# Kernel tuning notes

Measured on AMD Instinct MI355X. Metric: run time of the kernel, lower is better.

## Reference

```python
import jax, jax.numpy as jnp
import numpy as np

NUM_GROUPS = 4
NUM_HEADS = 8
EPS = 1e-5


def setup_inputs() -> dict:
    key = jax.random.key(0)
    k1, k2, k3 = jax.random.split(key, 3)
    B, C, D, H, W = 4, 256, 32, 32, 32
    x = jax.random.normal(k1, (B, C, D, H, W), dtype=jnp.float32)
    gn_weight = jnp.ones((C,), dtype=jnp.float32)
    gn_bias = jnp.zeros((C,), dtype=jnp.float32)
    # 1x1x1 conv weights collapse to [out_ch, in_ch] matrices
    qkv_weight = jax.random.normal(k2, (3 * C, C), dtype=jnp.float32) * (1.0 / np.sqrt(C))
    out_weight = jax.random.normal(k3, (C, C), dtype=jnp.float32) * (1.0 / np.sqrt(C))
    out_bias = jnp.zeros((C,), dtype=jnp.float32)
    return {"x": x, "gn_weight": gn_weight, "gn_bias": gn_bias,
            "qkv_weight": qkv_weight, "out_weight": out_weight, "out_bias": out_bias}


def _group_norm(x, weight, bias):
    B, C, D, H, W = x.shape
    g = NUM_GROUPS
    xg = x.reshape(B, g, C // g, D, H, W)
    mean = jnp.mean(xg, axis=(2, 3, 4, 5), keepdims=True)
    var = jnp.var(xg, axis=(2, 3, 4, 5), keepdims=True)
    xn = ((xg - mean) * jax.lax.rsqrt(var + EPS)).reshape(B, C, D, H, W)
    return xn * weight[None, :, None, None, None] + bias[None, :, None, None, None]


def reference(x, gn_weight, gn_bias, qkv_weight, out_weight, out_bias):
    B, C, D, H, W = x.shape
    N = D * H * W
    hd = C // NUM_HEADS  # per-head channels

    norm = _group_norm(x, gn_weight, gn_bias)
    # 1x1x1 conv == channel matmul: [B,3C,D,H,W]
    qkv = jnp.einsum('bcdhw,oc->bodhw', norm, qkv_weight)
    # 'b (qkv heads c) d h w -> qkv b heads c (d h w)'
    qkv = qkv.reshape(B, 3, NUM_HEADS, hd, N)
    q, k, v = qkv[:, 0], qkv[:, 1], qkv[:, 2]  # each [B, heads, hd, N]

    k = jax.nn.softmax(k, axis=-1)  # softmax over spatial dim
    sim = jnp.einsum('bhdn,bhen->bhde', k, v)   # [B, heads, hd, hd]
    out = jnp.einsum('bhde,bhdn->bhen', sim, q)  # [B, heads, hd, N]
    out = out.reshape(B, C, D, H, W)

    out = jnp.einsum('bcdhw,oc->bodhw', out, out_weight) + out_bias[None, :, None, None, None]
    return out + x
```

## Files before the change

### kernel.cpp

```cpp
#include <hip/hip_runtime.h>
#include <cmath>


typedef __bf16 bf16x8 __attribute__((ext_vector_type(8)));
typedef float f32x4 __attribute__((ext_vector_type(4)));

union U16 { uint4 u; unsigned short s[8]; bf16x8 v; };

__device__ __forceinline__ float bf2f(unsigned short h) {
    unsigned int u = ((unsigned int)h) << 16;
    return __builtin_bit_cast(float, u);
}
__device__ __forceinline__ unsigned short f2bf(float f) {
    unsigned int u = __builtin_bit_cast(unsigned int, f);
    u = (u + 0x7fffu + ((u >> 16) & 1u)) >> 16;
    return (unsigned short)u;
}
__device__ __forceinline__ unsigned int pack2(unsigned short a, unsigned short b) {
    return (unsigned int)a | ((unsigned int)b << 16);
}

__global__ __launch_bounds__(64) void k_detect(const unsigned int* __restrict__ xr,
                                               int* __restrict__ flag) {
    unsigned int u = xr[threadIdx.x * 997];
    int e = (u >> 7) & 0xFF;
    bool ok = (e >= 100) && (e <= 141);
    unsigned long long m = __ballot(ok);
    if (threadIdx.x == 0) *flag = (__popcll(m) < 32) ? 1 : 0;
}

__global__ __launch_bounds__(256) void k_cvt_w(const void* __restrict__ qkvw,
                                               const void* __restrict__ outw,
                                               const void* __restrict__ gnw,
                                               const void* __restrict__ gnb,
                                               const void* __restrict__ outb,
                                               const int* __restrict__ flagp,
                                               unsigned short* __restrict__ wdst) {
    int idx = blockIdx.x * 256 + threadIdx.x;
    if (idx >= 328448) return;
    int f = *flagp;
    const void* src; int off;
    if      (idx < 196608) { src = qkvw; off = idx; }
    else if (idx < 262144) { src = outw; off = idx - 196608; }
    else if (idx < 262400) { src = gnw;  off = idx - 262144; }
    else if (idx < 262656) { src = gnb;  off = idx - 262400; }
    else if (idx < 262912) { src = outb; off = idx - 262656; }
    else {
        int i = idx - 262912;
        int c = i >> 8, d = i & 255;
        src = qkvw; off = d * 256 + c;
    }
    wdst[idx] = f ? f2bf(((const float*)src)[off])
                  : ((const unsigned short*)src)[off];
}

__global__ __launch_bounds__(256) void k_gnsum(const void* __restrict__ xr,
                                               const int* __restrict__ flagp,
                                               float2* __restrict__ gn_part) {
    int t = threadIdx.x, bid = blockIdx.x;
    int grp = bid >> 7, chunk = bid & 127;
    size_t base = (size_t)grp * 2097152 + (size_t)chunk * 16384;
    int f = *flagp;
    float s = 0.f, q = 0.f;
    if (f) {
        const float* p = (const float*)xr + base;
        for (int i = 0; i < 8; i++) {
            float4 a = *(const float4*)(p + i * 2048 + t * 8);
            float4 b = *(const float4*)(p + i * 2048 + t * 8 + 4);
            float v[8] = {a.x, a.y, a.z, a.w, b.x, b.y, b.z, b.w};
#pragma unroll
            for (int j = 0; j < 8; j++) { s += v[j]; q += v[j] * v[j]; }
        }
    } else {
        const unsigned short* p = (const unsigned short*)xr + base;
        for (int i = 0; i < 8; i++) {
            U16 u; u.u = *(const uint4*)(p + i * 2048 + t * 8);
#pragma unroll
            for (int j = 0; j < 8; j++) { float v = bf2f(u.s[j]); s += v; q += v * v; }
        }
    }
#pragma unroll
    for (int off = 32; off > 0; off >>= 1) { s += __shfl_xor(s, off); q += __shfl_xor(q, off); }
    __shared__ float rs[4], rq[4];
    int wave = t >> 6;
    if ((t & 63) == 0) { rs[wave] = s; rq[wave] = q; }
    __syncthreads();
    if (t == 0) gn_part[bid] = make_float2(rs[0] + rs[1] + rs[2] + rs[3],
                                           rq[0] + rq[1] + rq[2] + rq[3]);
}

__global__ __launch_bounds__(128) void k_gnfinal(const float2* __restrict__ gn_part,
                                                 float2* __restrict__ gstats) {
    int bg = blockIdx.x, t = threadIdx.x;
    float2 v = gn_part[bg * 128 + t];
    float s = v.x, q = v.y;
#pragma unroll
    for (int off = 32; off > 0; off >>= 1) { s += __shfl_xor(s, off); q += __shfl_xor(q, off); }
    __shared__ float rs[2], rq[2];
    if ((t & 63) == 0) { rs[t >> 6] = s; rq[t >> 6] = q; }
    __syncthreads();
    if (t == 0) {
        const float inv = 1.0f / 2097152.0f;
        float S = rs[0] + rs[1], Q = rq[0] + rq[1];
        float mean = S * inv;
        float var = Q * inv - mean * mean;
        gstats[bg] = make_float2(mean, rsqrtf(var + 1e-5f));
    }
}

__global__ __launch_bounds__(64) void k_beta(const unsigned short* __restrict__ wq,
                                             const unsigned short* __restrict__ wgnw,
                                             const unsigned short* __restrict__ wgnb,
                                             const float2* __restrict__ gstats,
                                             float* __restrict__ beta) {
    int bid = blockIdx.x;
    int b = bid / 768, o = bid % 768;
    int t = threadIdx.x, c = t * 4;
    float2 ms = gstats[b * 4 + (c >> 6)];
    uint2 qw = *(const uint2*)(wq + o * 256 + c);
    uint2 gw = *(const uint2*)(wgnw + c);
    uint2 gb = *(const uint2*)(wgnb + c);
    unsigned short qs[4] = {(unsigned short)(qw.x & 0xffff), (unsigned short)(qw.x >> 16),
                            (unsigned short)(qw.y & 0xffff), (unsigned short)(qw.y >> 16)};
    unsigned short wsx[4] = {(unsigned short)(gw.x & 0xffff), (unsigned short)(gw.x >> 16),
                             (unsigned short)(gw.y & 0xffff), (unsigned short)(gw.y >> 16)};
    unsigned short bs[4] = {(unsigned short)(gb.x & 0xffff), (unsigned short)(gb.x >> 16),
                            (unsigned short)(gb.y & 0xffff), (unsigned short)(gb.y >> 16)};
    float bacc = 0.f;
#pragma unroll
    for (int j = 0; j < 4; j++)
        bacc += bf2f(qs[j]) * (bf2f(bs[j]) - ms.x * ms.y * bf2f(wsx[j]));
#pragma unroll
    for (int off = 32; off > 0; off >>= 1) bacc += __shfl_xor(bacc, off);
    if (t == 0) beta[b * 768 + o] = bacc;
}

__global__ __launch_bounds__(256) void k_cvt_t(const void* __restrict__ xr,
                                               const int* __restrict__ flagp,
                                               const unsigned short* __restrict__ wgnw,
                                               const float2* __restrict__ gstats,
                                               unsigned short* __restrict__ xt) {
    int tid = threadIdx.x, bid = blockIdx.x;
    int b = bid >> 11, r2 = bid & 2047, cblk = r2 >> 9, nblk = r2 & 511;
    float rstd = gstats[b * 4 + cblk].y;
    int f = *flagp;
    __shared__ __align__(16) unsigned short T[64 * 80];
    unsigned short tmp[2][8];
#pragma unroll
    for (int i = 0; i < 2; i++) {
        int crow = (tid >> 3) + 32 * i, nch = tid & 7;
        int c = cblk * 64 + crow;
        float sc = bf2f(wgnw[c]) * rstd;
        size_t base = ((size_t)(b * 256 + c)) * 32768 + (size_t)nblk * 64 + nch * 8;
        float v[8];
        if (f) {
            float4 a = *(const float4*)((const float*)xr + base);
            float4 d = *(const float4*)((const float*)xr + base + 4);
            v[0] = a.x; v[1] = a.y; v[2] = a.z; v[3] = a.w;
            v[4] = d.x; v[5] = d.y; v[6] = d.z; v[7] = d.w;
        } else {
            U16 u; u.u = *(const uint4*)((const unsigned short*)xr + base);
#pragma unroll
            for (int j = 0; j < 8; j++) v[j] = bf2f(u.s[j]);
        }
#pragma unroll
        for (int j = 0; j < 8; j++) tmp[i][j] = f2bf(v[j] * sc);
    }
#pragma unroll
    for (int i = 0; i < 2; i++) {
        int crow = (tid >> 3) + 32 * i, nch = tid & 7;
#pragma unroll
        for (int jj = 0; jj < 8; jj++) {
            int j = (jj + tid) & 7;
            T[(nch * 8 + j) * 80 + crow] = tmp[i][j];
        }
    }
    __syncthreads();
#pragma unroll
    for (int i = 0; i < 2; i++) {
        int nrow = (tid >> 3) + 32 * i, cch = tid & 7;
        uint4 v = *(const uint4*)&T[nrow * 80 + cch * 8];
        *(uint4*)(xt + ((size_t)b * 32768 + (size_t)nblk * 64 + nrow) * 256 + cblk * 64 + cch * 8) = v;
    }
}

__device__ __forceinline__ void stage_tile(const unsigned short* __restrict__ g, int stride,
                                           unsigned short* __restrict__ lds, int tid) {
    int lane = tid & 63, wave = tid >> 6;
    int r8 = lane >> 3, s = lane & 7;
#pragma unroll
    for (int i = 0; i < 4; i++) {
        int row0 = wave * 32 + i * 8;
        int row = row0 + r8;
        const unsigned short* src = g + (size_t)row * stride + ((s ^ (row & 7)) << 3);
        __builtin_amdgcn_global_load_lds(
            (__attribute__((address_space(1))) void*)src,
            (__attribute__((address_space(3))) void*)(lds + row0 * 64),
            16, 0, 0);
    }
}

__device__ __forceinline__ void mfma_tile(const unsigned short* __restrict__ ldsA,
                                          const unsigned short* __restrict__ ldsB,
                                          int l15, int quad, int wm, int wn,
                                          f32x4 (&acc)[4][4]) {
#pragma unroll
    for (int ks = 0; ks < 2; ks++) {
        bf16x8 af[4], bv[4];
#pragma unroll
        for (int mi = 0; mi < 4; mi++) {
            int row = wm * 64 + mi * 16 + l15;
            af[mi] = *(const bf16x8*)&ldsA[row * 64 + (((ks * 4 + quad) ^ (row & 7)) * 8)];
        }
#pragma unroll
        for (int ni = 0; ni < 4; ni++) {
            int row = wn * 64 + ni * 16 + l15;
            bv[ni] = *(const bf16x8*)&ldsB[row * 64 + (((ks * 4 + quad) ^ (row & 7)) * 8)];
        }
#pragma unroll
        for (int mi = 0; mi < 4; mi++)
#pragma unroll
            for (int ni = 0; ni < 4; ni++)
                acc[mi][ni] = __builtin_amdgcn_mfma_f32_16x16x32_bf16(af[mi], bv[ni], acc[mi][ni], 0, 0, 0);
    }
}

template<int KSTEPS, int KAMASK>
__device__ __forceinline__ void gemm_core_db(const unsigned short* __restrict__ A, int strideA,
                                             const unsigned short* __restrict__ B, int strideB,
                                             unsigned short* lds, int tid, f32x4 (&acc)[4][4]) {
    int lane = tid & 63, l15 = lane & 15, quad = lane >> 4;
    int wave = tid >> 6, wm = wave & 1, wn = wave >> 1;
    stage_tile(A, strideA, lds, tid);
    stage_tile(B, strideB, lds + 8192, tid);
    __syncthreads();
#pragma unroll
    for (int kt = 0; kt < KSTEPS; ++kt) {
        unsigned short* cur = lds + (kt & 1) * 16384;
        unsigned short* nxt = lds + (((kt & 1) ^ 1)) * 16384;
        if (kt + 1 < KSTEPS) {
            stage_tile(A + ((kt + 1) & KAMASK) * 64, strideA, nxt, tid);
            stage_tile(B + (kt + 1) * 64, strideB, nxt + 8192, tid);
        }
        mfma_tile(cur, cur + 8192, l15, quad, wm, wn, acc);
        __syncthreads();
    }
}

__global__ __launch_bounds__(256) void k_gemm1(const unsigned short* __restrict__ wq,
                                               const unsigned short* __restrict__ xt,
                                               const float* __restrict__ beta,
                                               unsigned short* __restrict__ kv,
                                               int b0) {
    __shared__ __align__(16) unsigned short ldsbuf[4 * 128 * 64];
    int tid = threadIdx.x, bid = blockIdx.x;
    int L = (bid & 7) * ((int)gridDim.x >> 3) + (bid >> 3);
    int mblk = L & 3;
    int t2 = L >> 2;
    int nblk = t2 & 255, bl = t2 >> 8;
    int gb = b0 + bl;
    int o0 = 256 + mblk * 128;
    size_t n0 = (size_t)nblk * 128;
    const unsigned short* A = wq + (size_t)o0 * 256;
    const unsigned short* B = xt + ((size_t)gb * 32768 + n0) * 256;
    f32x4 acc[4][4] = {};
    gemm_core_db<4, 3>(A, 256, B, 256, ldsbuf, tid, acc);

    int lane = tid & 63, l15 = lane & 15, quad = lane >> 4;
    int wave = tid >> 6, wm = wave & 1, wn = wave >> 1;
#pragma unroll
    for (int mi = 0; mi < 4; mi++) {
        int o_l = wm * 64 + mi * 16 + quad * 4;
        float4 be = *(const float4*)(beta + gb * 768 + o0 + o_l);
        float bev[4] = {be.x, be.y, be.z, be.w};
#pragma unroll
        for (int ni = 0; ni < 4; ni++) {
            int n_l = wn * 64 + ni * 16 + l15;
            f32x4 v = acc[mi][ni];
#pragma unroll
            for (int r = 0; r < 4; r++) {
                int o_r = o_l + r;
                ldsbuf[(o_r * 128 + n_l) ^ ((o_r & 7) << 3)] = f2bf(v[r] + bev[r]);
            }
        }
    }
    __syncthreads();
    int kv0 = mblk * 128;
#pragma unroll
    for (int p = 0; p < 8; p++) {
        int o_r = p * 16 + (tid >> 4);
        int ch = tid & 15;
        uint4 v = *(const uint4*)&ldsbuf[(o_r * 128 + ch * 8) ^ ((o_r & 7) << 3)];
        *(uint4*)(kv + ((size_t)bl * 512 + kv0 + o_r) * 32768 + n0 + ch * 8) = v;
    }
}

__global__ __launch_bounds__(256) void k_stats(const unsigned short* __restrict__ kv,
                                               float2* __restrict__ stats) {
    int row = blockIdx.x, t = threadIdx.x;
    const unsigned short* p = kv + ((size_t)(row >> 8) * 512 + (row & 255)) * 32768;
    float m = -3.0e38f;
    for (int i = 0; i < 16; i++) {
        U16 u; u.u = *(const uint4*)(p + i * 2048 + t * 8);
#pragma unroll
        for (int j = 0; j < 8; j++) m = fmaxf(m, bf2f(u.s[j]));
    }
#pragma unroll
    for (int off = 32; off > 0; off >>= 1) m = fmaxf(m, __shfl_xor(m, off));
    __shared__ float rm[4], rs[4];
    int wave = t >> 6;
    if ((t & 63) == 0) rm[wave] = m;
    __syncthreads();
    m = fmaxf(fmaxf(rm[0], rm[1]), fmaxf(rm[2], rm[3]));
    float s = 0.f;
    for (int i = 0; i < 16; i++) {
        U16 u; u.u = *(const uint4*)(p + i * 2048 + t * 8);
#pragma unroll
        for (int j = 0; j < 8; j++) s += __expf(bf2f(u.s[j]) - m);
    }
#pragma unroll
    for (int off = 32; off > 0; off >>= 1) s += __shfl_xor(s, off);
    if ((t & 63) == 0) rs[wave] = s;
    __syncthreads();
    if (t == 0) stats[row] = make_float2(m, 1.0f / (rs[0] + rs[1] + rs[2] + rs[3]));
}

__global__ __launch_bounds__(64) void k_sim(const unsigned short* __restrict__ kv,
                                            const float2* __restrict__ stats,
                                            float* __restrict__ partials) {
    int bid = blockIdx.x;
    int bh = bid >> 6, chunk = bid & 63;
    int b = bh >> 3, h = bh & 7;
    int lane = threadIdx.x, l15 = lane & 15, quad = lane >> 4;
    size_t n0 = (size_t)chunk * 512 + quad * 8;
    float mrow[2], isr[2];
#pragma unroll
    for (int mi = 0; mi < 2; mi++) {
        float2 st = stats[b * 256 + h * 32 + mi * 16 + l15];
        mrow[mi] = st.x; isr[mi] = st.y;
    }
    const unsigned short* kb = kv + ((size_t)b * 512 + h * 32) * 32768;
    const unsigned short* vb = kv + ((size_t)b * 512 + 256 + h * 32) * 32768;
    f32x4 acc[2][2] = {};
    for (int t = 0; t < 16; t++) {
        size_t n = n0 + t * 32;
        bf16x8 af[2], bv[2];
#pragma unroll
        for (int mi = 0; mi < 2; mi++) {
            U16 u; u.u = *(const uint4*)(kb + (size_t)(mi * 16 + l15) * 32768 + n);
            U16 pv;
#pragma unroll
            for (int j = 0; j < 8; j++) pv.s[j] = f2bf(__expf(bf2f(u.s[j]) - mrow[mi]) * isr[mi]);
            af[mi] = pv.v;
        }
#pragma unroll
        for (int ni = 0; ni < 2; ni++) {
            U16 u; u.u = *(const uint4*)(vb + (size_t)(ni * 16 + l15) * 32768 + n);
            bv[ni] = u.v;
        }
#pragma unroll
        for (int mi = 0; mi < 2; mi++)
#pragma unroll
            for (int ni = 0; ni < 2; ni++)
                acc[mi][ni] = __builtin_amdgcn_mfma_f32_16x16x32_bf16(af[mi], bv[ni], acc[mi][ni], 0, 0, 0);
    }
    float* po = partials + (size_t)(bh * 64 + chunk) * 1024;
#pragma unroll
    for (int mi = 0; mi < 2; mi++)
#pragma unroll
        for (int ni = 0; ni < 2; ni++)
#pragma unroll
            for (int rr = 0; rr < 4; rr++)
                po[(mi * 16 + quad * 4 + rr) * 32 + ni * 16 + l15] = acc[mi][ni][rr];
}

__global__ __launch_bounds__(256) void k_combine(const float* __restrict__ partials,
                                                 float* __restrict__ sim, int b0) {
    int bh = blockIdx.x, tid = threadIdx.x;
#pragma unroll
    for (int i = 0; i < 4; i++) {
        float a = 0.f;
        const float* p = partials + (size_t)bh * 65536 + tid + i * 256;
        for (int c = 0; c < 64; c++) a += p[(size_t)c * 1024];
        sim[(size_t)(b0 * 8 + bh) * 1024 + tid + i * 256] = a;
    }
}

__global__ __launch_bounds__(256) void k_buildM(const unsigned short* __restrict__ wo,
                                                const float* __restrict__ sim,
                                                const float* __restrict__ beta,
                                                const unsigned short* __restrict__ wob,
                                                unsigned short* __restrict__ M,
                                                float* __restrict__ gamma, int b0) {
    int bid = blockIdx.x, tid = threadIdx.x;
    int b = b0 + (bid >> 8), o = bid & 255;
    __shared__ float lw[256];
    __shared__ float ls[8192];
    lw[tid] = bf2f(wo[o * 256 + tid]);
#pragma unroll
    for (int i = 0; i < 32; i++) ls[tid + i * 256] = sim[(size_t)b * 8192 + tid + i * 256];
    __syncthreads();
    int h = tid >> 5, d = tid & 31;
    float a = 0.f;
#pragma unroll
    for (int e = 0; e < 32; e++) {
        int ee = (e + d) & 31;
        a += lw[h * 32 + ee] * ls[h * 1024 + d * 32 + ee];
    }
    unsigned short mh = f2bf(a);
    M[((size_t)b * 256 + o) * 256 + tid] = mh;
    float g = bf2f(mh) * beta[b * 768 + tid];
#pragma unroll
    for (int off = 32; off > 0; off >>= 1) g += __shfl_xor(g, off);
    __shared__ float rg[4];
    if ((tid & 63) == 0) rg[tid >> 6] = g;
    __syncthreads();
    if (tid == 0) gamma[b * 256 + o] = rg[0] + rg[1] + rg[2] + rg[3] + bf2f(wob[o]);
}

__global__ __launch_bounds__(256) void k_buildG(const unsigned short* __restrict__ M,
                                                const unsigned short* __restrict__ wqT,
                                                unsigned short* __restrict__ G2, int b0) {
    __shared__ __align__(16) unsigned short ldsbuf[4 * 128 * 64];
    int tid = threadIdx.x, bid = blockIdx.x;
    int b = b0 + (bid >> 2), t = bid & 3;
    int o0 = (t >> 1) * 128, c0 = (t & 1) * 128;
    const unsigned short* A = M + (size_t)b * 65536 + (size_t)o0 * 256;
    const unsigned short* B = wqT + (size_t)c0 * 256;
    f32x4 acc[4][4] = {};
    gemm_core_db<4, 3>(A, 256, B, 256, ldsbuf, tid, acc);

    int lane = tid & 63, l15 = lane & 15, quad = lane >> 4;
    int wave = tid >> 6, wm = wave & 1, wn = wave >> 1;
#pragma unroll
    for (int mi = 0; mi < 4; mi++) {
        int o_l = o0 + wm * 64 + mi * 16 + quad * 4;
#pragma unroll
        for (int ni = 0; ni < 4; ni++) {
            int c_l = c0 + wn * 64 + ni * 16 + l15;
            f32x4 v = acc[mi][ni];
#pragma unroll
            for (int r = 0; r < 4; r++) {
                float g = v[r];
                unsigned short hi = f2bf(g);
                unsigned short lo = f2bf(g - bf2f(hi));
                size_t rb = (size_t)b * 131072 + (size_t)(o_l + r) * 512 + c_l;
                G2[rb] = hi;
                G2[rb + 256] = lo;
            }
        }
    }
}

__global__ __launch_bounds__(256) void k_gemm2(const unsigned short* __restrict__ xt,
                                               const unsigned short* __restrict__ G2,
                                               const float* __restrict__ gamma,
                                               const void* __restrict__ xr,
                                               const int* __restrict__ flagp,
                                               void* __restrict__ outv) {
    __shared__ __align__(16) unsigned short ldsbuf[4 * 128 * 64];
    float* ldsF = (float*)ldsbuf;
    int tid = threadIdx.x, bid = blockIdx.x;
    int L = (bid & 7) * ((int)gridDim.x >> 3) + (bid >> 3);
    int oblk = L & 1;
    int mblk = (L >> 1) & 255;
    int b = L >> 9;
    size_t n0 = (size_t)mblk * 128;
    int o0 = oblk * 128;
    const unsigned short* A = xt + ((size_t)b * 32768 + n0) * 256;
    const unsigned short* Bg = G2 + (size_t)b * 131072 + (size_t)o0 * 512;
    f32x4 acc[4][4] = {};
    gemm_core_db<8, 3>(A, 256, Bg, 512, ldsbuf, tid, acc);

    int f = *flagp;
    int lane = tid & 63, l15 = lane & 15, quad = lane >> 4;
    int wave = tid >> 6, wm = wave & 1, wn = wave >> 1;
    for (int half = 0; half < 2; half++) {
        if (wn == half) {
#pragma unroll
            for (int mi = 0; mi < 4; mi++) {
#pragma unroll
                for (int ni = 0; ni < 4; ni++) {
                    int o_h = ni * 16 + l15;
                    f32x4 v = acc[mi][ni];
#pragma unroll
                    for (int r = 0; r < 4; r++) {
                        int n_l = wm * 64 + mi * 16 + quad * 4 + r;
                        ldsF[(o_h * 128 + n_l) ^ ((o_h & 15) << 2)] = v[r];
                    }
                }
            }
        }
        __syncthreads();
#pragma unroll
        for (int p = 0; p < 8; p++) {
            int o_h = p * 8 + (tid >> 5);
            int ch = tid & 31;
            float4 v = *(const float4*)&ldsF[(o_h * 128 + ch * 4) ^ ((o_h & 15) << 2)];
            int o = o0 + half * 64 + o_h;
            float bias = gamma[b * 256 + o];
            size_t base = ((size_t)b * 256 + o) * 32768 + n0 + ch * 4;
            if (f) {
                float4 xv = *(const float4*)((const float*)xr + base);
                float4 ov = make_float4(v.x + bias + xv.x, v.y + bias + xv.y,
                                        v.z + bias + xv.z, v.w + bias + xv.w);
                *(float4*)((float*)outv + base) = ov;
            } else {
                uint2 xr2 = *(const uint2*)((const unsigned short*)xr + base);
                unsigned short xs[4] = {(unsigned short)(xr2.x & 0xffff), (unsigned short)(xr2.x >> 16),
                                        (unsigned short)(xr2.y & 0xffff), (unsigned short)(xr2.y >> 16)};
                uint2 pv;
                pv.x = pack2(f2bf(v.x + bias + bf2f(xs[0])), f2bf(v.y + bias + bf2f(xs[1])));
                pv.y = pack2(f2bf(v.z + bias + bf2f(xs[2])), f2bf(v.w + bias + bf2f(xs[3])));
                *(uint2*)((unsigned short*)outv + base) = pv;
            }
        }
        __syncthreads();
    }
}

extern "C" void kernel_launch(void* const* d_in, const int* in_sizes, int n_in,
                              void* d_out, int out_size, void* d_ws, size_t ws_size,
                              hipStream_t stream) {
    const void* x    = d_in[0];
    const void* gnw  = d_in[1];
    const void* gnb  = d_in[2];
    const void* qkvw = d_in[3];
    const void* outw = d_in[4];
    const void* outb = d_in[5];
    char* ws = (char*)d_ws;

    unsigned short* xt   = (unsigned short*)(ws);
    unsigned short* wdst = (unsigned short*)(ws + 67108864);
    char* sm = ws + 68157440;
    int*    flag    = (int*)(sm);
    float2* gstats  = (float2*)(sm + 64);
    float*  beta    = (float*)(sm + 1024);
    float2* stats   = (float2*)(sm + 16384);
    float*  gamma   = (float*)(sm + 24576);
    float2* gn_part = (float2*)(sm + 32768);
    float*  sim     = (float*)(sm + 65536);
    unsigned short* M  = (unsigned short*)(sm + 262144);
    unsigned short* G2 = (unsigned short*)(sm + 786432);
    const size_t kv_off = 70254592;

    const unsigned short* wq   = wdst;
    const unsigned short* wo   = wdst + 196608;
    const unsigned short* wgnw = wdst + 262144;
    const unsigned short* wgnb = wdst + 262400;
    const unsigned short* wob  = wdst + 262656;
    const unsigned short* wqT  = wdst + 262912;

    int nb = 1;
    if      (ws_size >= kv_off + 4ull * (33554432 + 2097152)) nb = 4;
    else if (ws_size >= kv_off + 2ull * (33554432 + 2097152)) nb = 2;

    unsigned short* kv = (unsigned short*)(ws + kv_off);
    float* partials    = (float*)(ws + kv_off + (size_t)nb * 33554432);

    k_detect <<<dim3(1),    dim3(64),  0, stream>>>((const unsigned int*)x, flag);
    k_cvt_w  <<<dim3(1283), dim3(256), 0, stream>>>(qkvw, outw, gnw, gnb, outb, flag, wdst);
    k_gnsum  <<<dim3(2048), dim3(256), 0, stream>>>(x, flag, gn_part);
    k_gnfinal<<<dim3(16),   dim3(128), 0, stream>>>(gn_part, gstats);
    k_beta   <<<dim3(3072), dim3(64),  0, stream>>>(wq, wgnw, wgnb, gstats, beta);
    k_cvt_t  <<<dim3(8192), dim3(256), 0, stream>>>(x, flag, wgnw, gstats, xt);

    for (int pass = 0; pass < 4; pass += nb) {
        k_gemm1  <<<dim3(1024 * nb), dim3(256), 0, stream>>>(wq, xt, beta, kv, pass);
        k_stats  <<<dim3(256 * nb),  dim3(256), 0, stream>>>(kv, stats);
        k_sim    <<<dim3(512 * nb),  dim3(64),  0, stream>>>(kv, stats, partials);
        k_combine<<<dim3(8 * nb),    dim3(256), 0, stream>>>(partials, sim, pass);
        k_buildM <<<dim3(256 * nb),  dim3(256), 0, stream>>>(wo, sim, beta, wob, M, gamma, pass);
        k_buildG <<<dim3(4 * nb),    dim3(256), 0, stream>>>(M, wqT, G2, pass);
    }
    k_gemm2<<<dim3(2048), dim3(256), 0, stream>>>(xt, G2, gamma, x, flag, d_out);
}
```

Measured before the change: 510.3 us.

## Make GEMM blocks loop over multiple N tiles and pack k_sim waves per block

```diff
diff --git a/kernel.cpp b/kernel.cpp
--- a/kernel.cpp
+++ b/kernel.cpp
@@ -252,46 +252,66 @@
                                                const float* __restrict__ beta,
                                                unsigned short* __restrict__ kv,
                                                int b0) {
-    __shared__ __align__(16) unsigned short ldsbuf[4 * 128 * 64];
+    __shared__ __align__(16) unsigned short lds[4 * 8192];
     int tid = threadIdx.x, bid = blockIdx.x;
-    int L = (bid & 7) * ((int)gridDim.x >> 3) + (bid >> 3);
+    int cpx = (int)gridDim.x >> 3;
+    int L = (bid & 7) * cpx + (bid >> 3);
     int mblk = L & 3;
-    int t2 = L >> 2;
-    int nblk = t2 & 255, bl = t2 >> 8;
+    int ngrp = (L >> 2) & 127;
+    int bl = L >> 9;
     int gb = b0 + bl;
     int o0 = 256 + mblk * 128;
-    size_t n0 = (size_t)nblk * 128;
     const unsigned short* A = wq + (size_t)o0 * 256;
-    const unsigned short* B = xt + ((size_t)gb * 32768 + n0) * 256;
-    f32x4 acc[4][4] = {};
-    gemm_core_db<4, 3>(A, 256, B, 256, ldsbuf, tid, acc);
-
+    const unsigned short* Bb = xt + ((size_t)gb * 32768 + (size_t)ngrp * 256) * 256;
     int lane = tid & 63, l15 = lane & 15, quad = lane >> 4;
     int wave = tid >> 6, wm = wave & 1, wn = wave >> 1;
-#pragma unroll
-    for (int mi = 0; mi < 4; mi++) {
-        int o_l = wm * 64 + mi * 16 + quad * 4;
-        float4 be = *(const float4*)(beta + gb * 768 + o0 + o_l);
-        float bev[4] = {be.x, be.y, be.z, be.w};
-#pragma unroll
-        for (int ni = 0; ni < 4; ni++) {
-            int n_l = wn * 64 + ni * 16 + l15;
-            f32x4 v = acc[mi][ni];
-#pragma unroll
-            for (int r = 0; r < 4; r++) {
-                int o_r = o_l + r;
-                ldsbuf[(o_r * 128 + n_l) ^ ((o_r & 7) << 3)] = f2bf(v[r] + bev[r]);
+    int kv0 = mblk * 128;
+
+    stage_tile(A, 256, lds, tid);
+    stage_tile(Bb, 256, lds + 8192, tid);
+    __syncthreads();
+    for (int t = 0; t < 2; ++t) {
+        f32x4 acc[4][4] = {};
+#pragma unroll
+        for (int kt = 0; kt < 4; ++kt) {
+            int g = t * 4 + kt;
+            unsigned short* cur = lds + (g & 1) * 16384;
+            unsigned short* nxt = lds + ((g + 1) & 1) * 16384;
+            if (g + 1 < 8) {
+                int g2 = g + 1, t2 = g2 >> 2, k2 = g2 & 3;
+                stage_tile(A + k2 * 64, 256, nxt, tid);
+                stage_tile(Bb + ((size_t)t2 * 128) * 256 + k2 * 64, 256, nxt + 8192, tid);
             }
-        }
-    }
-    __syncthreads();
-    int kv0 = mblk * 128;
-#pragma unroll
-    for (int p = 0; p < 8; p++) {
-        int o_r = p * 16 + (tid >> 4);
-        int ch = tid & 15;
-        uint4 v = *(const uint4*)&ldsbuf[(o_r * 128 + ch * 8) ^ ((o_r & 7) << 3)];
-        *(uint4*)(kv + ((size_t)bl * 512 + kv0 + o_r) * 32768 + n0 + ch * 8) = v;
+            mfma_tile(cur, cur + 8192, l15, quad, wm, wn, acc);
+            __syncthreads();
+        }
+        unsigned short* scr = lds + 16384;
+        size_t n0 = ((size_t)ngrp * 2 + t) * 128;
+#pragma unroll
+        for (int mi = 0; mi < 4; mi++) {
+            int o_l = wm * 64 + mi * 16 + quad * 4;
+            float4 be = *(const float4*)(beta + gb * 768 + o0 + o_l);
+            float bev[4] = {be.x, be.y, be.z, be.w};
+#pragma unroll
+            for (int ni = 0; ni < 4; ni++) {
+                int n_l = wn * 64 + ni * 16 + l15;
+                f32x4 v = acc[mi][ni];
+#pragma unroll
+                for (int r = 0; r < 4; r++) {
+                    int o_r = o_l + r;
+                    scr[(o_r * 128 + n_l) ^ ((o_r & 7) << 3)] = f2bf(v[r] + bev[r]);
+                }
+            }
+        }
+        __syncthreads();
+#pragma unroll
+        for (int p = 0; p < 8; p++) {
+            int o_r = p * 16 + (tid >> 4);
+            int ch = tid & 15;
+            uint4 v = *(const uint4*)&scr[(o_r * 128 + ch * 8) ^ ((o_r & 7) << 3)];
+            *(uint4*)(kv + ((size_t)bl * 512 + kv0 + o_r) * 32768 + n0 + ch * 8) = v;
+        }
+        __syncthreads();
     }
 }
 
@@ -325,13 +345,14 @@
     if (t == 0) stats[row] = make_float2(m, 1.0f / (rs[0] + rs[1] + rs[2] + rs[3]));
 }
 
-__global__ __launch_bounds__(64) void k_sim(const unsigned short* __restrict__ kv,
-                                            const float2* __restrict__ stats,
-                                            float* __restrict__ partials) {
+__global__ __launch_bounds__(256) void k_sim(const unsigned short* __restrict__ kv,
+                                             const float2* __restrict__ stats,
+                                             float* __restrict__ partials) {
     int bid = blockIdx.x;
-    int bh = bid >> 6, chunk = bid & 63;
+    int bh = bid >> 4;
+    int chunk = (bid & 15) * 4 + (threadIdx.x >> 6);
     int b = bh >> 3, h = bh & 7;
-    int lane = threadIdx.x, l15 = lane & 15, quad = lane >> 4;
+    int lane = threadIdx.x & 63, l15 = lane & 15, quad = lane >> 4;
     size_t n0 = (size_t)chunk * 512 + quad * 8;
     float mrow[2], isr[2];
 #pragma unroll
@@ -421,7 +442,7 @@
 __global__ __launch_bounds__(256) void k_buildG(const unsigned short* __restrict__ M,
                                                 const unsigned short* __restrict__ wqT,
                                                 unsigned short* __restrict__ G2, int b0) {
-    __shared__ __align__(16) unsigned short ldsbuf[4 * 128 * 64];
+    __shared__ __align__(16) unsigned short ldsbuf[4 * 8192];
     int tid = threadIdx.x, bid = blockIdx.x;
     int b = b0 + (bid >> 2), t = bid & 3;
     int o0 = (t >> 1) * 128, c0 = (t & 1) * 128;
@@ -458,64 +479,82 @@
                                                const void* __restrict__ xr,
                                                const int* __restrict__ flagp,
                                                void* __restrict__ outv) {
-    __shared__ __align__(16) unsigned short ldsbuf[4 * 128 * 64];
-    float* ldsF = (float*)ldsbuf;
+    __shared__ __align__(16) unsigned short lds[4 * 8192];
     int tid = threadIdx.x, bid = blockIdx.x;
-    int L = (bid & 7) * ((int)gridDim.x >> 3) + (bid >> 3);
+    int cpx = (int)gridDim.x >> 3;
+    int L = (bid & 7) * cpx + (bid >> 3);
     int oblk = L & 1;
-    int mblk = (L >> 1) & 255;
-    int b = L >> 9;
-    size_t n0 = (size_t)mblk * 128;
+    int ngrp = (L >> 1) & 63;
+    int b = L >> 7;
     int o0 = oblk * 128;
-    const unsigned short* A = xt + ((size_t)b * 32768 + n0) * 256;
+    const unsigned short* Ab = xt + ((size_t)b * 32768 + (size_t)ngrp * 512) * 256;
     const unsigned short* Bg = G2 + (size_t)b * 131072 + (size_t)o0 * 512;
-    f32x4 acc[4][4] = {};
-    gemm_core_db<8, 3>(A, 256, Bg, 512, ldsbuf, tid, acc);
-
-    int f = *flagp;
     int lane = tid & 63, l15 = lane & 15, quad = lane >> 4;
     int wave = tid >> 6, wm = wave & 1, wn = wave >> 1;
-    for (int half = 0; half < 2; half++) {
-        if (wn == half) {
-#pragma unroll
-            for (int mi = 0; mi < 4; mi++) {
-#pragma unroll
-                for (int ni = 0; ni < 4; ni++) {
-                    int o_h = ni * 16 + l15;
-                    f32x4 v = acc[mi][ni];
-#pragma unroll
-                    for (int r = 0; r < 4; r++) {
-                        int n_l = wm * 64 + mi * 16 + quad * 4 + r;
-                        ldsF[(o_h * 128 + n_l) ^ ((o_h & 15) << 2)] = v[r];
+    int f = *flagp;
+
+    stage_tile(Ab, 256, lds, tid);
+    stage_tile(Bg, 512, lds + 8192, tid);
+    __syncthreads();
+    for (int t = 0; t < 4; ++t) {
+        f32x4 acc[4][4] = {};
+#pragma unroll
+        for (int kt = 0; kt < 8; ++kt) {
+            int g = t * 8 + kt;
+            unsigned short* cur = lds + (g & 1) * 16384;
+            unsigned short* nxt = lds + ((g + 1) & 1) * 16384;
+            if (g + 1 < 32) {
+                int g2 = g + 1, t2 = g2 >> 3, k2 = g2 & 7;
+                stage_tile(Ab + ((size_t)t2 * 128) * 256 + (k2 & 3) * 64, 256, nxt, tid);
+                stage_tile(Bg + k2 * 64, 512, nxt + 8192, tid);
+            }
+            mfma_tile(cur, cur + 8192, l15, quad, wm, wn, acc);
+            __syncthreads();
+        }
+        float* ldsF = (float*)(lds + 16384);
+        size_t n0 = ((size_t)ngrp * 4 + t) * 128;
+        for (int half = 0; half < 2; half++) {
+            if (wn == half) {
+#pragma unroll
+                for (int mi = 0; mi < 4; mi++) {
+#pragma unroll
+                    for (int ni = 0; ni < 4; ni++) {
+                        int o_h = ni * 16 + l15;
+                        f32x4 v = acc[mi][ni];
+#pragma unroll
+                        for (int r = 0; r < 4; r++) {
+                            int n_l = wm * 64 + mi * 16 + quad * 4 + r;
+                            ldsF[(o_h * 128 + n_l) ^ ((o_h & 15) << 2)] = v[r];
+                        }
                     }
                 }
             }
-        }
-        __syncthreads();
-#pragma unroll
-        for (int p = 0; p < 8; p++) {
-            int o_h = p * 8 + (tid >> 5);
-            int ch = tid & 31;
-            float4 v = *(const float4*)&ldsF[(o_h * 128 + ch * 4) ^ ((o_h & 15) << 2)];
-            int o = o0 + half * 64 + o_h;
-            float bias = gamma[b * 256 + o];
-            size_t base = ((size_t)b * 256 + o) * 32768 + n0 + ch * 4;
-            if (f) {
-                float4 xv = *(const float4*)((const float*)xr + base);
-                float4 ov = make_float4(v.x + bias + xv.x, v.y + bias + xv.y,
-                                        v.z + bias + xv.z, v.w + bias + xv.w);
-                *(float4*)((float*)outv + base) = ov;
-            } else {
-                uint2 xr2 = *(const uint2*)((const unsigned short*)xr + base);
-                unsigned short xs[4] = {(unsigned short)(xr2.x & 0xffff), (unsigned short)(xr2.x >> 16),
-                                        (unsigned short)(xr2.y & 0xffff), (unsigned short)(xr2.y >> 16)};
-                uint2 pv;
-                pv.x = pack2(f2bf(v.x + bias + bf2f(xs[0])), f2bf(v.y + bias + bf2f(xs[1])));
-                pv.y = pack2(f2bf(v.z + bias + bf2f(xs[2])), f2bf(v.w + bias + bf2f(xs[3])));
-                *(uint2*)((unsigned short*)outv + base) = pv;
+            __syncthreads();
+#pragma unroll
+            for (int p = 0; p < 8; p++) {
+                int o_h = p * 8 + (tid >> 5);
+                int ch = tid & 31;
+                float4 v = *(const float4*)&ldsF[(o_h * 128 + ch * 4) ^ ((o_h & 15) << 2)];
+                int o = o0 + half * 64 + o_h;
+                float bias = gamma[b * 256 + o];
+                size_t base = ((size_t)b * 256 + o) * 32768 + n0 + ch * 4;
+                if (f) {
+                    float4 xv = *(const float4*)((const float*)xr + base);
+                    float4 ov = make_float4(v.x + bias + xv.x, v.y + bias + xv.y,
+                                            v.z + bias + xv.z, v.w + bias + xv.w);
+                    *(float4*)((float*)outv + base) = ov;
+                } else {
+                    uint2 xr2 = *(const uint2*)((const unsigned short*)xr + base);
+                    unsigned short xs[4] = {(unsigned short)(xr2.x & 0xffff), (unsigned short)(xr2.x >> 16),
+                                            (unsigned short)(xr2.y & 0xffff), (unsigned short)(xr2.y >> 16)};
+                    uint2 pv;
+                    pv.x = pack2(f2bf(v.x + bias + bf2f(xs[0])), f2bf(v.y + bias + bf2f(xs[1])));
+                    pv.y = pack2(f2bf(v.z + bias + bf2f(xs[2])), f2bf(v.w + bias + bf2f(xs[3])));
+                    *(uint2*)((unsigned short*)outv + base) = pv;
+                }
             }
-        }
-        __syncthreads();
+            __syncthreads();
+        }
     }
 }
 
@@ -566,12 +605,12 @@
     k_cvt_t  <<<dim3(8192), dim3(256), 0, stream>>>(x, flag, wgnw, gstats, xt);
 
     for (int pass = 0; pass < 4; pass += nb) {
-        k_gemm1  <<<dim3(1024 * nb), dim3(256), 0, stream>>>(wq, xt, beta, kv, pass);
-        k_stats  <<<dim3(256 * nb),  dim3(256), 0, stream>>>(kv, stats);
-        k_sim    <<<dim3(512 * nb),  dim3(64),  0, stream>>>(kv, stats, partials);
-        k_combine<<<dim3(8 * nb),    dim3(256), 0, stream>>>(partials, sim, pass);
-        k_buildM <<<dim3(256 * nb),  dim3(256), 0, stream>>>(wo, sim, beta, wob, M, gamma, pass);
-        k_buildG <<<dim3(4 * nb),    dim3(256), 0, stream>>>(M, wqT, G2, pass);
-    }
-    k_gemm2<<<dim3(2048), dim3(256), 0, stream>>>(xt, G2, gamma, x, flag, d_out);
-}
+        k_gemm1  <<<dim3(512 * nb), dim3(256), 0, stream>>>(wq, xt, beta, kv, pass);
+        k_stats  <<<dim3(256 * nb), dim3(256), 0, stream>>>(kv, stats);
+        k_sim    <<<dim3(128 * nb), dim3(256), 0, stream>>>(kv, stats, partials);
+        k_combine<<<dim3(8 * nb),   dim3(256), 0, stream>>>(partials, sim, pass);
+        k_buildM <<<dim3(256 * nb), dim3(256), 0, stream>>>(wo, sim, beta, wob, M, gamma, pass);
+        k_buildG <<<dim3(4 * nb),   dim3(256), 0, stream>>>(M, wqT, G2, pass);
+    }
+    k_gemm2<<<dim3(512), dim3(256), 0, stream>>>(xt, G2, gamma, x, flag, d_out);
+}
```

New measurement: 574.6 us. 1.13x slower.
